# Performance work log

Hardware: AMD Instinct MI355X
Metric: run time of the kernel (lower is better)

Reference implementation:

```python
import jax, jax.numpy as jnp
import numpy as np

B, T, D = 32, 2048, 256   # batch, encoder time steps, input_dim
H = 256                   # output_dim (GRU hidden)
A = 128                   # attention_dim
C = 4367                  # nb_classes
STEPS = 22                # max_out_t_steps


def setup_inputs() -> dict:
    key = jax.random.key(0)
    ks = jax.random.split(key, 11)
    s = 0.05
    return {
        "x": jax.random.normal(ks[0], (B, T, D), dtype=jnp.float32),
        # additive attention params: softmax_T(tanh(x Wx + h Wh) @ v)
        "Wx": jax.random.normal(ks[1], (D, A), dtype=jnp.float32) * s,
        "Wh": jax.random.normal(ks[2], (H, A), dtype=jnp.float32) * s,
        "v": jax.random.normal(ks[3], (A,), dtype=jnp.float32) * s,
        # torch GRUCell params
        "W_ih": jax.random.normal(ks[4], (3 * H, D), dtype=jnp.float32) * s,
        "W_hh": jax.random.normal(ks[5], (3 * H, H), dtype=jnp.float32) * s,
        "b_ih": jax.random.normal(ks[6], (3 * H,), dtype=jnp.float32) * s,
        "b_hh": jax.random.normal(ks[7], (3 * H,), dtype=jnp.float32) * s,
        # classifier
        "W_cls": jax.random.normal(ks[8], (C, H), dtype=jnp.float32) * s,
        "b_cls": jax.random.normal(ks[9], (C,), dtype=jnp.float32) * s,
    }


def reference(x, Wx, Wh, v, W_ih, W_hh, b_ih, b_hh, W_cls, b_cls):
    # dropout layers are identity in eval/reference mode
    xW = jnp.einsum("btd,da->bta", x, Wx)  # hoisted: constant across steps
    h0 = jnp.zeros((x.shape[0], H), dtype=x.dtype)

    def step(h, _):
        # additive attention over time axis
        e = jnp.einsum("bta,a->bt", jnp.tanh(xW + (h @ Wh)[:, None, :]), v)
        att = jax.nn.softmax(e, axis=1)          # [B, T]
        ctx = jnp.einsum("btd,bt->bd", x, att)   # weighted sum over T
        # torch GRUCell
        gi = ctx @ W_ih.T + b_ih                  # [B, 3H]
        gh = h @ W_hh.T + b_hh                    # [B, 3H]
        i_r, i_z, i_n = jnp.split(gi, 3, axis=1)
        h_r, h_z, h_n = jnp.split(gh, 3, axis=1)
        r = jax.nn.sigmoid(i_r + h_r)
        z = jax.nn.sigmoid(i_z + h_z)
        n = jnp.tanh(i_n + r * h_n)
        h_new = (1.0 - z) * n + z * h
        logits = h_new @ W_cls.T + b_cls          # [B, C]
        return h_new, logits

    _, outs = jax.lax.scan(step, h0, None, length=STEPS)  # [STEPS, B, C]
    return jnp.transpose(outs, (1, 0, 2))                 # [B, STEPS, C]
```

## Files before the change

kernel.cpp:

```cpp
#include <hip/hip_runtime.h>

#define BB 32
#define TT 2048
#define DD 256
#define HH 256
#define AA 128
#define CC 4367
#define CLS_LD 4480
#define NSTEPS 22
#define NCHUNK 32

typedef unsigned short ushortT;
typedef unsigned int uintT;
typedef unsigned long long u64T;
using frag8 = __attribute__((ext_vector_type(8))) short;
using f32x4 = __attribute__((ext_vector_type(4))) float;

__device__ __forceinline__ float tanh_fast(float u) {
  float e = __expf(2.0f * u);
  return 1.0f - 2.0f / (e + 1.0f);
}
__device__ __forceinline__ float sigmoid_fast(float u) {
  return 1.0f / (1.0f + __expf(-u));
}
__device__ __forceinline__ ushortT f2bf(float f) {
  unsigned int u = __float_as_uint(f);
  unsigned int r = (u + 0x7FFFu + ((u >> 16) & 1u)) >> 16;
  return (ushortT)r;
}
__device__ __forceinline__ float bf2f(ushortT v) {
  return __uint_as_float(((unsigned int)v) << 16);
}

__global__ __launch_bounds__(256) void trans_kernel(
    const float* __restrict__ Wx, const float* __restrict__ W_cls,
    float* __restrict__ WclsT, ushortT* __restrict__ WxT_bf) {
  int blk = blockIdx.x;
  __shared__ float tile[32][33];
  const int li = threadIdx.x >> 5, lj = threadIdx.x & 31;
  if (blk < 1096) {
    int i0 = (blk >> 3) * 32, j0 = (blk & 7) * 32;
#pragma unroll
    for (int k = 0; k < 4; ++k) {
      int i = i0 + li + k * 8;
      if (i < CC) tile[li + k * 8][lj] = W_cls[(size_t)i * 256 + j0 + lj];
    }
    __syncthreads();
#pragma unroll
    for (int k = 0; k < 4; ++k) {
      int j = j0 + li + k * 8, i = i0 + lj;
      if (i < CC) WclsT[(size_t)j * CLS_LD + i] = tile[lj][li + k * 8];
    }
  } else {
    blk -= 1096;
    int i0 = (blk >> 2) * 32, j0 = (blk & 3) * 32;
#pragma unroll
    for (int k = 0; k < 4; ++k)
      tile[li + k * 8][lj] = Wx[(size_t)(i0 + li + k * 8) * 128 + j0 + lj];
    __syncthreads();
#pragma unroll
    for (int k = 0; k < 4; ++k) {
      int j = j0 + li + k * 8;
      WxT_bf[(size_t)j * 256 + i0 + lj] = f2bf(tile[lj][li + k * 8]);
    }
  }
}

__global__ __launch_bounds__(256) void xw_mfma(
    const float* __restrict__ x, const ushortT* __restrict__ WxT_bf,
    ushortT* __restrict__ x_bf, ushortT* __restrict__ xW_ta) {
  __shared__ ushortT lds[2 * 128 * 72];
#define SX(r, c) lds[(r) * 72 + (c)]
#define SW(r, c) lds[128 * 72 + (r) * 72 + (c)]
#define ST(m, a) lds[(m) * 136 + (a)]
  const int tid = threadIdx.x;
  const int lane = tid & 63, w = tid >> 6;
  const int l15 = lane & 15, quad = lane >> 4;
  const int r0 = blockIdx.x * 128;
  const int row = tid >> 1, half = tid & 1;

  f32x4 acc[2][8];
#pragma unroll
  for (int mt = 0; mt < 2; ++mt)
#pragma unroll
    for (int nt = 0; nt < 8; ++nt) acc[mt][nt] = (f32x4){0.f, 0.f, 0.f, 0.f};

  for (int kk0 = 0; kk0 < 256; kk0 += 64) {
    {
      const float4* xp = (const float4*)(x + (size_t)(r0 + row) * DD + kk0 + half * 32);
      uint4 pk[4];
#pragma unroll
      for (int i = 0; i < 4; ++i) {
        float4 f0 = xp[2 * i], f1 = xp[2 * i + 1];
        pk[i].x = (uintT)f2bf(f0.x) | ((uintT)f2bf(f0.y) << 16);
        pk[i].y = (uintT)f2bf(f0.z) | ((uintT)f2bf(f0.w) << 16);
        pk[i].z = (uintT)f2bf(f1.x) | ((uintT)f2bf(f1.y) << 16);
        pk[i].w = (uintT)f2bf(f1.z) | ((uintT)f2bf(f1.w) << 16);
      }
      uint4* sxp = (uint4*)&SX(row, half * 32);
      uint4* gxp = (uint4*)(x_bf + (size_t)(r0 + row) * DD + kk0 + half * 32);
#pragma unroll
      for (int i = 0; i < 4; ++i) { sxp[i] = pk[i]; gxp[i] = pk[i]; }
    }
    {
      const uint4* wp = (const uint4*)(WxT_bf + (size_t)row * DD + kk0 + half * 32);
      uint4* swp = (uint4*)&SW(row, half * 32);
#pragma unroll
      for (int i = 0; i < 4; ++i) swp[i] = wp[i];
    }
    __syncthreads();
#pragma unroll
    for (int kk = 0; kk < 2; ++kk) {
      frag8 a0 = *(const frag8*)&SX(w * 32 + l15, kk * 32 + quad * 8);
      frag8 a1 = *(const frag8*)&SX(w * 32 + 16 + l15, kk * 32 + quad * 8);
#pragma unroll
      for (int nt = 0; nt < 8; ++nt) {
        frag8 bf = *(const frag8*)&SW(nt * 16 + l15, kk * 32 + quad * 8);
        acc[0][nt] = __builtin_amdgcn_mfma_f32_16x16x32_bf16(a0, bf, acc[0][nt], 0, 0, 0);
        acc[1][nt] = __builtin_amdgcn_mfma_f32_16x16x32_bf16(a1, bf, acc[1][nt], 0, 0, 0);
      }
    }
    __syncthreads();
  }
#pragma unroll
  for (int mt = 0; mt < 2; ++mt)
#pragma unroll
    for (int nt = 0; nt < 8; ++nt)
#pragma unroll
      for (int r = 0; r < 4; ++r) {
        int m = w * 32 + mt * 16 + quad * 4 + r;
        int a = nt * 16 + l15;
        ST(m, a) = f2bf(acc[mt][nt][r]);
      }
  __syncthreads();
  {
    const uint4* sp = (const uint4*)&ST(row, half * 64);
    uint4* gp = (uint4*)(xW_ta + (size_t)(r0 + row) * AA + half * 64);
#pragma unroll
    for (int i = 0; i < 8; ++i) gp[i] = sp[i];
  }
#undef SX
#undef SW
#undef ST
}

__global__ __launch_bounds__(256) void gates_kernel(
    const float* __restrict__ ctx_part, const float* __restrict__ den_part,
    const float* __restrict__ hall, const float* __restrict__ W_ih,
    const float* __restrict__ W_hh, const float* __restrict__ b_ih,
    const float* __restrict__ b_hh, float* __restrict__ gi_buf,
    float* __restrict__ gh_buf, int s) {
  const int slice = blockIdx.x, b = blockIdx.y, tid = threadIdx.x;
  __shared__ __align__(16) float sctx[DD];
  __shared__ float sden;
  if (tid < 32) {
    float d = den_part[b * NCHUNK + tid];
#pragma unroll
    for (int off = 16; off > 0; off >>= 1) d += __shfl_down(d, off, 32);
    if (tid == 0) sden = d;
  }
  {
    float acc = 0.f;
#pragma unroll
    for (int c = 0; c < NCHUNK; ++c)
      acc += ctx_part[((size_t)b * NCHUNK + c) * DD + tid];
    sctx[tid] = acc;
  }
  __syncthreads();
  const float invd = 1.0f / sden;
  const int kq = tid & 15, gsub = tid >> 4;
  const float4* cp = (const float4*)sctx + kq * 4;
  const float4* hrow = (s >= 2) ? (const float4*)(hall + ((size_t)(s - 2) * BB + b) * HH) + kq * 4 : nullptr;
  float4 c4[4], h4[4];
#pragma unroll
  for (int j = 0; j < 4; ++j) {
    float4 cv = cp[j];
    c4[j].x = cv.x * invd; c4[j].y = cv.y * invd; c4[j].z = cv.z * invd; c4[j].w = cv.w * invd;
    if (hrow) h4[j] = hrow[j];
    else { h4[j].x = 0.f; h4[j].y = 0.f; h4[j].z = 0.f; h4[j].w = 0.f; }
  }
#pragma unroll
  for (int it = 0; it < 3; ++it) {
    const int g = slice * 48 + it * 16 + gsub;
    const float4* wi = (const float4*)(W_ih + (size_t)g * DD) + kq * 4;
    const float4* wh = (const float4*)(W_hh + (size_t)g * HH) + kq * 4;
    float gi = 0.f, gh = 0.f;
#pragma unroll
    for (int j = 0; j < 4; ++j) {
      float4 wv = wi[j];
      gi += c4[j].x * wv.x + c4[j].y * wv.y + c4[j].z * wv.z + c4[j].w * wv.w;
      wv = wh[j];
      gh += h4[j].x * wv.x + h4[j].y * wv.y + h4[j].z * wv.z + h4[j].w * wv.w;
    }
#pragma unroll
    for (int off = 8; off > 0; off >>= 1) {
      gi += __shfl_down(gi, off, 16);
      gh += __shfl_down(gh, off, 16);
    }
    if (kq == 0) {
      gi_buf[b * 768 + g] = gi + b_ih[g];
      gh_buf[b * 768 + g] = gh + b_hh[g];
    }
  }
}

__global__ __launch_bounds__(256) void hcomb_kernel(
    const float* __restrict__ gi_buf, const float* __restrict__ gh_buf,
    const float* __restrict__ Wh, float* __restrict__ hall,
    float* __restrict__ hWh_buf, int s) {
  const int b = blockIdx.x, as = blockIdx.y, i = threadIdx.x;
  __shared__ float sh[HH];
  __shared__ float part[8][32];
  {
    float gir = gi_buf[b * 768 + i], giz = gi_buf[b * 768 + 256 + i], gin = gi_buf[b * 768 + 512 + i];
    float ghr = gh_buf[b * 768 + i], ghz = gh_buf[b * 768 + 256 + i], ghn = gh_buf[b * 768 + 512 + i];
    float hp = (s >= 2) ? hall[((size_t)(s - 2) * BB + b) * HH + i] : 0.f;
    float r = sigmoid_fast(gir + ghr);
    float z = sigmoid_fast(giz + ghz);
    float n = tanh_fast(gin + r * ghn);
    float hv = (1.f - z) * n + z * hp;
    if (as == 0) hall[((size_t)(s - 1) * BB + b) * HH + i] = hv;
    sh[i] = hv;
  }
  __syncthreads();
  {
    const int a = i & 31, kq = i >> 5;
    const int ga = as * 32 + a;
    float acc = 0.f;
#pragma unroll
    for (int k = kq * 32; k < kq * 32 + 32; ++k)
      acc = fmaf(sh[k], Wh[k * AA + ga], acc);
    part[kq][a] = acc;
  }
  __syncthreads();
  if (i < 32) {
    float sum = part[0][i] + part[1][i] + part[2][i] + part[3][i]
              + part[4][i] + part[5][i] + part[6][i] + part[7][i];
    hWh_buf[b * AA + as * 32 + i] = sum;
  }
}

__global__ __launch_bounds__(256, 4) void att_kernel(
    const ushortT* __restrict__ x_bf, const ushortT* __restrict__ xW_ta,
    const float* __restrict__ hWh_buf, const float* __restrict__ v,
    float* __restrict__ ctx_part, float* __restrict__ den_part) {
  const int tid = threadIdx.x;
  const int b = blockIdx.x;
  const int chunk = blockIdx.y;
  const int t0 = chunk * 64;
  __shared__ float sh_hWh[AA], sh_v[AA];
  __shared__ float sh_w[64];
  __shared__ __align__(16) float sh_ctx[4 * DD];
  if (tid < AA) {
    sh_hWh[tid] = hWh_buf ? hWh_buf[b * AA + tid] : 0.f;
    sh_v[tid] = v[tid];
  }
  __syncthreads();
  const int j4 = tid >> 6, dq = tid & 63;
  u64T xr[16];
  {
    const u64T* xb4 = (const u64T*)x_bf;
#pragma unroll
    for (int j = 0; j < 16; ++j)
      xr[j] = __builtin_nontemporal_load(
          &xb4[(((size_t)(b * TT + t0 + j * 4 + j4)) * DD >> 2) + dq]);
  }
  {
    const int tl = tid >> 2, aseg = tid & 3;
    const uint4* xw16 = (const uint4*)(xW_ta + (size_t)(b * TT + t0 + tl) * AA + aseg * 32);
    float e = 0.f;
#pragma unroll
    for (int i = 0; i < 4; ++i) {
      uint4 u = xw16[i];
      const int ab = aseg * 32 + i * 8;
      e = fmaf(tanh_fast(bf2f((ushortT)(u.x & 0xFFFFu)) + sh_hWh[ab + 0]), sh_v[ab + 0], e);
      e = fmaf(tanh_fast(bf2f((ushortT)(u.x >> 16)) + sh_hWh[ab + 1]), sh_v[ab + 1], e);
      e = fmaf(tanh_fast(bf2f((ushortT)(u.y & 0xFFFFu)) + sh_hWh[ab + 2]), sh_v[ab + 2], e);
      e = fmaf(tanh_fast(bf2f((ushortT)(u.y >> 16)) + sh_hWh[ab + 3]), sh_v[ab + 3], e);
      e = fmaf(tanh_fast(bf2f((ushortT)(u.z & 0xFFFFu)) + sh_hWh[ab + 4]), sh_v[ab + 4], e);
      e = fmaf(tanh_fast(bf2f((ushortT)(u.z >> 16)) + sh_hWh[ab + 5]), sh_v[ab + 5], e);
      e = fmaf(tanh_fast(bf2f((ushortT)(u.w & 0xFFFFu)) + sh_hWh[ab + 6]), sh_v[ab + 6], e);
      e = fmaf(tanh_fast(bf2f((ushortT)(u.w >> 16)) + sh_hWh[ab + 7]), sh_v[ab + 7], e);
    }
    e += __shfl_xor(e, 1, 4);
    e += __shfl_xor(e, 2, 4);
    if (aseg == 0) sh_w[tl] = __expf(e);
  }
  __syncthreads();
  {
    float4 acc = {0.f, 0.f, 0.f, 0.f};
#pragma unroll
    for (int j = 0; j < 16; ++j) {
      float w = sh_w[j * 4 + j4];
      u64T u = xr[j];
      acc.x = fmaf(w, bf2f((ushortT)(u       & 0xFFFFu)), acc.x);
      acc.y = fmaf(w, bf2f((ushortT)((u >> 16) & 0xFFFFu)), acc.y);
      acc.z = fmaf(w, bf2f((ushortT)((u >> 32) & 0xFFFFu)), acc.z);
      acc.w = fmaf(w, bf2f((ushortT)((u >> 48) & 0xFFFFu)), acc.w);
    }
    ((float4*)sh_ctx)[j4 * 64 + dq] = acc;
  }
  __syncthreads();
  {
    float sum = sh_ctx[tid] + sh_ctx[DD + tid] + sh_ctx[2 * DD + tid] + sh_ctx[3 * DD + tid];
    ctx_part[((size_t)b * NCHUNK + chunk) * DD + tid] = sum;
  }
  if (tid < 64) {
    float ds = sh_w[tid];
#pragma unroll
    for (int off = 32; off > 0; off >>= 1) ds += __shfl_down(ds, off, 64);
    if (tid == 0) den_part[b * NCHUNK + chunk] = ds;
  }
}

__global__ __launch_bounds__(256) void cls_kernel(
    const float* __restrict__ hall, const float* __restrict__ WclsT,
    const float* __restrict__ b_cls, float* __restrict__ out) {
  const int tid = threadIdx.x;
  const int c0 = blockIdx.x * 128;
  const int r0 = blockIdx.y * 32;
  const int cq = tid & 31, rg = tid >> 5;
  const int c = c0 + cq * 4;
  __shared__ __align__(16) float shh[32 * HH];
  {
    const float4* hsrc = (const float4*)(hall + (size_t)r0 * HH);
    float4* hdst = (float4*)shh;
#pragma unroll
    for (int i = 0; i < 8; ++i) hdst[tid + 256 * i] = hsrc[tid + 256 * i];
  }
  __syncthreads();
  float acc[4][4];
#pragma unroll
  for (int j = 0; j < 4; ++j)
#pragma unroll
    for (int l = 0; l < 4; ++l) acc[j][l] = 0.f;
#pragma unroll 4
  for (int k = 0; k < HH; ++k) {
    float4 w4 = *(const float4*)(WclsT + (size_t)k * CLS_LD + c);
    float h0 = shh[(rg * 4 + 0) * HH + k];
    float h1 = shh[(rg * 4 + 1) * HH + k];
    float h2 = shh[(rg * 4 + 2) * HH + k];
    float h3 = shh[(rg * 4 + 3) * HH + k];
    acc[0][0] = fmaf(h0, w4.x, acc[0][0]); acc[0][1] = fmaf(h0, w4.y, acc[0][1]);
    acc[0][2] = fmaf(h0, w4.z, acc[0][2]); acc[0][3] = fmaf(h0, w4.w, acc[0][3]);
    acc[1][0] = fmaf(h1, w4.x, acc[1][0]); acc[1][1] = fmaf(h1, w4.y, acc[1][1]);
    acc[1][2] = fmaf(h1, w4.z, acc[1][2]); acc[1][3] = fmaf(h1, w4.w, acc[1][3]);
    acc[2][0] = fmaf(h2, w4.x, acc[2][0]); acc[2][1] = fmaf(h2, w4.y, acc[2][1]);
    acc[2][2] = fmaf(h2, w4.z, acc[2][2]); acc[2][3] = fmaf(h2, w4.w, acc[2][3]);
    acc[3][0] = fmaf(h3, w4.x, acc[3][0]); acc[3][1] = fmaf(h3, w4.y, acc[3][1]);
    acc[3][2] = fmaf(h3, w4.z, acc[3][2]); acc[3][3] = fmaf(h3, w4.w, acc[3][3]);
  }
#pragma unroll
  for (int j = 0; j < 4; ++j) {
    int row = r0 + rg * 4 + j;
    int bb = row & (BB - 1), st = row >> 5;
    size_t obase = ((size_t)bb * NSTEPS + st) * CC;
#pragma unroll
    for (int l = 0; l < 4; ++l) {
      int cc = c + l;
      if (cc < CC) out[obase + cc] = acc[j][l] + b_cls[cc];
    }
  }
}

extern "C" void kernel_launch(void* const* d_in, const int* in_sizes, int n_in,
                              void* d_out, int out_size, void* d_ws, size_t ws_size,
                              hipStream_t stream) {
  const float* x     = (const float*)d_in[0];
  const float* Wx    = (const float*)d_in[1];
  const float* Wh    = (const float*)d_in[2];
  const float* v     = (const float*)d_in[3];
  const float* W_ih  = (const float*)d_in[4];
  const float* W_hh  = (const float*)d_in[5];
  const float* b_ih  = (const float*)d_in[6];
  const float* b_hh  = (const float*)d_in[7];
  const float* W_cls = (const float*)d_in[8];
  const float* b_cls = (const float*)d_in[9];
  float* out = (float*)d_out;

  float* ctx_part = (float*)d_ws;
  float* den_part = ctx_part + (size_t)BB * NCHUNK * DD;
  float* hWh_buf  = den_part + BB * NCHUNK;
  float* gi_buf   = hWh_buf + BB * AA;
  float* gh_buf   = gi_buf + BB * 768;
  float* hall     = gh_buf + BB * 768;
  float* WclsT    = hall + (size_t)NSTEPS * BB * HH;
  ushortT* WxT_bf = (ushortT*)(WclsT + (size_t)256 * CLS_LD);
  ushortT* x_bf   = WxT_bf + 128 * 256;
  ushortT* xW_ta  = x_bf + (size_t)BB * TT * DD;

  trans_kernel<<<1096 + 32, 256, 0, stream>>>(Wx, W_cls, WclsT, WxT_bf);
  xw_mfma<<<(BB * TT) / 128, 256, 0, stream>>>(x, WxT_bf, x_bf, xW_ta);

  att_kernel<<<dim3(BB, NCHUNK), 256, 0, stream>>>(x_bf, xW_ta, nullptr, v, ctx_part, den_part);
  for (int s = 1; s < NSTEPS; ++s) {
    gates_kernel<<<dim3(16, BB), 256, 0, stream>>>(ctx_part, den_part, hall, W_ih, W_hh,
                                                   b_ih, b_hh, gi_buf, gh_buf, s);
    hcomb_kernel<<<dim3(BB, 4), 256, 0, stream>>>(gi_buf, gh_buf, Wh, hall, hWh_buf, s);
    att_kernel<<<dim3(BB, NCHUNK), 256, 0, stream>>>(x_bf, xW_ta, hWh_buf, v, ctx_part, den_part);
  }
  gates_kernel<<<dim3(16, BB), 256, 0, stream>>>(ctx_part, den_part, hall, W_ih, W_hh,
                                                 b_ih, b_hh, gi_buf, gh_buf, NSTEPS);
  hcomb_kernel<<<dim3(BB, 4), 256, 0, stream>>>(gi_buf, gh_buf, Wh, hall, hWh_buf, NSTEPS);
  cls_kernel<<<dim3(35, 22), 256, 0, stream>>>(hall, WclsT, b_cls, out);
}
```

Measured before the change: 632.4 us.

## Fuse GRU gate combine and h·Wh projection into gates kernel

Gate rows are regrouped so each block computes the r, z and n rows for the same 16 hidden units. The block then applies the GRU update itself and emits a partial h·Wh over its 16 units. The attention kernel sums the 16 partials when it loads hWh. This drops one kernel launch per step and the gi/gh round trip through global memory. In exchange, att_kernel does extra reads to reduce the partials, and the h·Wh work is spread thinly across blocks.

```diff
diff --git a/kernel.cpp b/kernel.cpp
--- a/kernel.cpp
+++ b/kernel.cpp
@@ -146,13 +146,14 @@
 
 __global__ __launch_bounds__(256) void gates_kernel(
     const float* __restrict__ ctx_part, const float* __restrict__ den_part,
-    const float* __restrict__ hall, const float* __restrict__ W_ih,
+    const float* __restrict__ hall_c, const float* __restrict__ W_ih,
     const float* __restrict__ W_hh, const float* __restrict__ b_ih,
-    const float* __restrict__ b_hh, float* __restrict__ gi_buf,
-    float* __restrict__ gh_buf, int s) {
-  const int slice = blockIdx.x, b = blockIdx.y, tid = threadIdx.x;
+    const float* __restrict__ b_hh, const float* __restrict__ Wh,
+    float* __restrict__ hall, float* __restrict__ hWh_part, int s) {
+  const int sl = blockIdx.x, b = blockIdx.y, tid = threadIdx.x;
   __shared__ __align__(16) float sctx[DD];
   __shared__ float sden;
+  __shared__ float sh16[16];
   if (tid < 32) {
     float d = den_part[b * NCHUNK + tid];
 #pragma unroll
@@ -170,7 +171,7 @@
   const float invd = 1.0f / sden;
   const int kq = tid & 15, gsub = tid >> 4;
   const float4* cp = (const float4*)sctx + kq * 4;
-  const float4* hrow = (s >= 2) ? (const float4*)(hall + ((size_t)(s - 2) * BB + b) * HH) + kq * 4 : nullptr;
+  const float4* hrow = (s >= 2) ? (const float4*)(hall_c + ((size_t)(s - 2) * BB + b) * HH) + kq * 4 : nullptr;
   float4 c4[4], h4[4];
 #pragma unroll
   for (int j = 0; j < 4; ++j) {
@@ -179,9 +180,10 @@
     if (hrow) h4[j] = hrow[j];
     else { h4[j].x = 0.f; h4[j].y = 0.f; h4[j].z = 0.f; h4[j].w = 0.f; }
   }
+  float gi_g[3], gh_g[3];
 #pragma unroll
   for (int it = 0; it < 3; ++it) {
-    const int g = slice * 48 + it * 16 + gsub;
+    const int g = it * 256 + sl * 16 + gsub;
     const float4* wi = (const float4*)(W_ih + (size_t)g * DD) + kq * 4;
     const float4* wh = (const float4*)(W_hh + (size_t)g * HH) + kq * 4;
     float gi = 0.f, gh = 0.f;
@@ -197,52 +199,32 @@
       gi += __shfl_down(gi, off, 16);
       gh += __shfl_down(gh, off, 16);
     }
-    if (kq == 0) {
-      gi_buf[b * 768 + g] = gi + b_ih[g];
-      gh_buf[b * 768 + g] = gh + b_hh[g];
-    }
-  }
-}
-
-__global__ __launch_bounds__(256) void hcomb_kernel(
-    const float* __restrict__ gi_buf, const float* __restrict__ gh_buf,
-    const float* __restrict__ Wh, float* __restrict__ hall,
-    float* __restrict__ hWh_buf, int s) {
-  const int b = blockIdx.x, as = blockIdx.y, i = threadIdx.x;
-  __shared__ float sh[HH];
-  __shared__ float part[8][32];
-  {
-    float gir = gi_buf[b * 768 + i], giz = gi_buf[b * 768 + 256 + i], gin = gi_buf[b * 768 + 512 + i];
-    float ghr = gh_buf[b * 768 + i], ghz = gh_buf[b * 768 + 256 + i], ghn = gh_buf[b * 768 + 512 + i];
-    float hp = (s >= 2) ? hall[((size_t)(s - 2) * BB + b) * HH + i] : 0.f;
-    float r = sigmoid_fast(gir + ghr);
-    float z = sigmoid_fast(giz + ghz);
-    float n = tanh_fast(gin + r * ghn);
+    gi_g[it] = gi + b_ih[g];
+    gh_g[it] = gh + b_hh[g];
+  }
+  if (kq == 0) {
+    const int i = sl * 16 + gsub;
+    float hp = (s >= 2) ? hall_c[((size_t)(s - 2) * BB + b) * HH + i] : 0.f;
+    float r = sigmoid_fast(gi_g[0] + gh_g[0]);
+    float z = sigmoid_fast(gi_g[1] + gh_g[1]);
+    float n = tanh_fast(gi_g[2] + r * gh_g[2]);
     float hv = (1.f - z) * n + z * hp;
-    if (as == 0) hall[((size_t)(s - 1) * BB + b) * HH + i] = hv;
-    sh[i] = hv;
-  }
-  __syncthreads();
-  {
-    const int a = i & 31, kq = i >> 5;
-    const int ga = as * 32 + a;
+    hall[((size_t)(s - 1) * BB + b) * HH + i] = hv;
+    sh16[gsub] = hv;
+  }
+  __syncthreads();
+  if (tid < AA) {
     float acc = 0.f;
 #pragma unroll
-    for (int k = kq * 32; k < kq * 32 + 32; ++k)
-      acc = fmaf(sh[k], Wh[k * AA + ga], acc);
-    part[kq][a] = acc;
-  }
-  __syncthreads();
-  if (i < 32) {
-    float sum = part[0][i] + part[1][i] + part[2][i] + part[3][i]
-              + part[4][i] + part[5][i] + part[6][i] + part[7][i];
-    hWh_buf[b * AA + as * 32 + i] = sum;
+    for (int k = 0; k < 16; ++k)
+      acc = fmaf(sh16[k], Wh[(size_t)(sl * 16 + k) * AA + tid], acc);
+    hWh_part[((size_t)b * 16 + sl) * AA + tid] = acc;
   }
 }
 
 __global__ __launch_bounds__(256, 4) void att_kernel(
     const ushortT* __restrict__ x_bf, const ushortT* __restrict__ xW_ta,
-    const float* __restrict__ hWh_buf, const float* __restrict__ v,
+    const float* __restrict__ hWh_part, const float* __restrict__ v,
     float* __restrict__ ctx_part, float* __restrict__ den_part) {
   const int tid = threadIdx.x;
   const int b = blockIdx.x;
@@ -252,7 +234,13 @@
   __shared__ float sh_w[64];
   __shared__ __align__(16) float sh_ctx[4 * DD];
   if (tid < AA) {
-    sh_hWh[tid] = hWh_buf ? hWh_buf[b * AA + tid] : 0.f;
+    float hw = 0.f;
+    if (hWh_part) {
+#pragma unroll
+      for (int sl = 0; sl < 16; ++sl)
+        hw += hWh_part[((size_t)b * 16 + sl) * AA + tid];
+    }
+    sh_hWh[tid] = hw;
     sh_v[tid] = v[tid];
   }
   __syncthreads();
@@ -380,10 +368,8 @@
 
   float* ctx_part = (float*)d_ws;
   float* den_part = ctx_part + (size_t)BB * NCHUNK * DD;
-  float* hWh_buf  = den_part + BB * NCHUNK;
-  float* gi_buf   = hWh_buf + BB * AA;
-  float* gh_buf   = gi_buf + BB * 768;
-  float* hall     = gh_buf + BB * 768;
+  float* hWh_part = den_part + BB * NCHUNK;
+  float* hall     = hWh_part + (size_t)BB * 16 * AA;
   float* WclsT    = hall + (size_t)NSTEPS * BB * HH;
   ushortT* WxT_bf = (ushortT*)(WclsT + (size_t)256 * CLS_LD);
   ushortT* x_bf   = WxT_bf + 128 * 256;
@@ -393,14 +379,11 @@
   xw_mfma<<<(BB * TT) / 128, 256, 0, stream>>>(x, WxT_bf, x_bf, xW_ta);
 
   att_kernel<<<dim3(BB, NCHUNK), 256, 0, stream>>>(x_bf, xW_ta, nullptr, v, ctx_part, den_part);
-  for (int s = 1; s < NSTEPS; ++s) {
+  for (int s = 1; s <= NSTEPS; ++s) {
     gates_kernel<<<dim3(16, BB), 256, 0, stream>>>(ctx_part, den_part, hall, W_ih, W_hh,
-                                                   b_ih, b_hh, gi_buf, gh_buf, s);
-    hcomb_kernel<<<dim3(BB, 4), 256, 0, stream>>>(gi_buf, gh_buf, Wh, hall, hWh_buf, s);
-    att_kernel<<<dim3(BB, NCHUNK), 256, 0, stream>>>(x_bf, xW_ta, hWh_buf, v, ctx_part, den_part);
-  }
-  gates_kernel<<<dim3(16, BB), 256, 0, stream>>>(ctx_part, den_part, hall, W_ih, W_hh,
-                                                 b_ih, b_hh, gi_buf, gh_buf, NSTEPS);
-  hcomb_kernel<<<dim3(BB, 4), 256, 0, stream>>>(gi_buf, gh_buf, Wh, hall, hWh_buf, NSTEPS);
+                                                   b_ih, b_hh, Wh, hall, hWh_part, s);
+    if (s < NSTEPS)
+      att_kernel<<<dim3(BB, NCHUNK), 256, 0, stream>>>(x_bf, xW_ta, hWh_part, v, ctx_part, den_part);
+  }
   cls_kernel<<<dim3(35, 22), 256, 0, stream>>>(hall, WclsT, b_cls, out);
 }
```

Result: faster. 598.9 us (-5.3%).
